# Performance work log

Hardware: AMD Instinct MI355X
Metric: run time of the kernel (lower is better)

## Reference

```python
import jax, jax.numpy as jnp
import numpy as np

# dims
H = 2048      # hidden_size
NH = 16       # num q heads
NKV = 8       # num kv heads
D = 128       # head_dim
E = 16        # routed experts
K = 4         # top_k
I = 1024      # moe_intermediate_size (per routed expert)
SI = 1024     # shared expert intermediate (moe_intermediate * num_shared)
T = 2048      # tokens
EPS = 1e-5
THETA = 10000.0
RSF = 1.0     # router_scaling_factor


def setup_inputs() -> dict:
    key = jax.random.key(0)
    ks = jax.random.split(key, 10)
    s = 0.02
    return {
        "positions": jnp.arange(T, dtype=jnp.int32),
        "hidden_states": jax.random.normal(ks[0], (T, H), jnp.float32),
        "qkv_w": jax.random.normal(ks[1], (H, (NH + 2 * NKV) * D), jnp.float32) * s,
        "o_w": jax.random.normal(ks[2], (NH * D, H), jnp.float32) * s,
        "q_norm_w": jnp.ones((D,), jnp.float32),
        "k_norm_w": jnp.ones((D,), jnp.float32),
        "ln1_w": jnp.ones((H,), jnp.float32),
        "ln2_w": jnp.ones((H,), jnp.float32),
        "gate_w": jax.random.normal(ks[3], (H, E), jnp.float32) * s,
        "expert_bias": jax.random.normal(ks[4], (E,), jnp.float32) * 0.1,
        "shared_gu_w": jax.random.normal(ks[5], (H, 2 * SI), jnp.float32) * s,
        "shared_down_w": jax.random.normal(ks[6], (SI, H), jnp.float32) * s,
        "exp_gu_w": jax.random.normal(ks[7], (E, H, 2 * I), jnp.float32) * s,
        "exp_down_w": jax.random.normal(ks[8], (E, I, H), jnp.float32) * s,
    }


def _rmsnorm(x, w):
    v = jnp.mean(x * x, axis=-1, keepdims=True)
    return x * jax.lax.rsqrt(v + EPS) * w


def _rope(x, cos, sin):
    # neox style: rotate halves. x: [T, heads, D]; cos/sin: [T, 1, D//2]
    x1, x2 = x[..., : D // 2], x[..., D // 2 :]
    return jnp.concatenate([x1 * cos - x2 * sin, x2 * cos + x1 * sin], axis=-1)


def reference(positions, hidden_states, qkv_w, o_w, q_norm_w, k_norm_w,
              ln1_w, ln2_w, gate_w, expert_bias, shared_gu_w, shared_down_w,
              exp_gu_w, exp_down_w):
    hs = hidden_states
    # --- attention block ---
    x = _rmsnorm(hs, ln1_w)
    qkv = x @ qkv_w
    q = qkv[:, : NH * D].reshape(T, NH, D)
    k = qkv[:, NH * D : NH * D + NKV * D].reshape(T, NKV, D)
    v = qkv[:, NH * D + NKV * D :].reshape(T, NKV, D)
    # per-head qk RMSNorm
    q = _rmsnorm(q, q_norm_w)
    k = _rmsnorm(k, k_norm_w)
    # rotary embedding
    inv_freq = 1.0 / (THETA ** (jnp.arange(0, D, 2, dtype=jnp.float32) / D))
    ang = positions.astype(jnp.float32)[:, None] * inv_freq  # [T, D/2]
    cos = jnp.cos(ang)[:, None, :]
    sin = jnp.sin(ang)[:, None, :]
    q = _rope(q, cos, sin)
    k = _rope(k, cos, sin)
    # GQA: repeat kv heads
    rep = NH // NKV
    k = jnp.repeat(k, rep, axis=1)  # [T, NH, D]
    v = jnp.repeat(v, rep, axis=1)
    scores = jnp.einsum('qhd,khd->hqk', q, k) * (D ** -0.5)
    causal = jnp.tril(jnp.ones((T, T), dtype=bool))
    scores = jnp.where(causal[None], scores, -1e30)
    attn = jax.nn.softmax(scores, axis=-1)
    ao = jnp.einsum('hqk,khd->qhd', attn, v).reshape(T, NH * D)
    h = hs + ao @ o_w
    # --- MoE block ---
    x2 = _rmsnorm(h, ln2_w)
    router_logits = x2 @ gate_w  # fp32 gate
    sig = jax.nn.sigmoid(router_logits)
    biased = sig + expert_bias  # correction bias only used for selection
    _, top_idx = jax.lax.top_k(biased, K)  # [T, K]
    w = jnp.take_along_axis(sig, top_idx, axis=-1)
    w = w / jnp.sum(w, axis=-1, keepdims=True) * RSF  # renormalize + routed scaling
    combine = jnp.sum(jax.nn.one_hot(top_idx, E, dtype=x2.dtype) * w[..., None], axis=1)  # [T, E]
    # routed experts (dense-masked reference for the grouped GEMM)
    gu = jnp.einsum('th,ehi->eti', x2, exp_gu_w)  # [E, T, 2I]
    act = jax.nn.silu(gu[..., :I]) * gu[..., I:]
    routed = jnp.einsum('eti,eih->eth', act, exp_down_w)
    routed = jnp.einsum('eth,te->th', routed, combine)
    # shared expert
    sgu = x2 @ shared_gu_w
    shared = (jax.nn.silu(sgu[:, :SI]) * sgu[:, SI:]) @ shared_down_w
    return h + routed + shared
```

## Files before the change

### kernel.cpp

```cpp
#include <hip/hip_runtime.h>
#include <math.h>

#define T_ 2048
#define H_ 2048
#define NH_ 16
#define NKV_ 8
#define D_ 128
#define E_ 16
#define I_ 1024
#define SI_ 1024

typedef _Float16 half8 __attribute__((ext_vector_type(8)));
typedef _Float16 half4_t __attribute__((ext_vector_type(4)));
typedef float f32x4 __attribute__((ext_vector_type(4)));

#define MFMA32(a,b,c) __builtin_amdgcn_mfma_f32_16x16x32_f16((a),(b),(c),0,0,0)

__device__ __constant__ float LO_S = 2048.0f;
__device__ __constant__ float LO_I = 1.0f/2048.0f;
#define EPS_ 1e-5f

#define GL16(gp, lp) __builtin_amdgcn_global_load_lds( \
    (const __attribute__((address_space(1))) unsigned int*)(const void*)(gp), \
    (__attribute__((address_space(3))) unsigned int*)(void*)(lp), 16, 0, 0)

__global__ void tables_k(const int* __restrict__ pos, float* __restrict__ cosT, float* __restrict__ sinT) {
  int t = blockIdx.x;
  int j = threadIdx.x;
  float pf = (float)pow(10000.0, (double)j / 64.0);
  float invf = 1.0f / pf;
  float ang = (float)pos[t] * invf;
  cosT[t*64 + j] = (float)cos((double)ang);
  sinT[t*64 + j] = (float)sin((double)ang);
}

__global__ __launch_bounds__(256) void rmsnorm_k(const float* __restrict__ x, const float* __restrict__ w,
                                                 _Float16* __restrict__ oh, _Float16* __restrict__ ol) {
  int row = blockIdx.x;
  const float* xr = x + (size_t)row * H_;
  int tid = threadIdx.x;
  float4 a = *(const float4*)(xr + tid*8);
  float4 b = *(const float4*)(xr + tid*8 + 4);
  float ss = a.x*a.x + a.y*a.y + a.z*a.z + a.w*a.w + b.x*b.x + b.y*b.y + b.z*b.z + b.w*b.w;
  #pragma unroll
  for (int m = 1; m < 64; m <<= 1) ss += __shfl_xor(ss, m);
  __shared__ float wsum[4];
  int wid = tid >> 6, lane = tid & 63;
  if (lane == 0) wsum[wid] = ss;
  __syncthreads();
  float tot = wsum[0] + wsum[1] + wsum[2] + wsum[3];
  float rinv = 1.0f / sqrtf(tot / (float)H_ + EPS_);
  const float* av = (const float*)&a;
  const float* bv = (const float*)&b;
  #pragma unroll
  for (int j = 0; j < 8; ++j) {
    float xv = (j < 4) ? av[j] : bv[j-4];
    float val = xv * rinv * w[tid*8 + j];
    _Float16 h = (_Float16)val;
    size_t o = (size_t)row*H_ + tid*8 + j;
    oh[o] = h;
    ol[o] = (_Float16)((val - (float)h) * LO_S);
  }
}

__global__ __launch_bounds__(128) void qkvpost_k(
    const float* __restrict__ qkv, const float* __restrict__ qnw, const float* __restrict__ knw,
    const float* __restrict__ cosT, const float* __restrict__ sinT,
    _Float16* __restrict__ qh, _Float16* __restrict__ ql,
    _Float16* __restrict__ kh, _Float16* __restrict__ kl,
    _Float16* __restrict__ vth, _Float16* __restrict__ vtl) {
  int t = blockIdx.x, u = blockIdx.y, d = threadIdx.x;
  float val = qkv[(size_t)t*4096 + u*128 + d];
  __shared__ float sv[128];
  __shared__ float ssum[2];
  if (u < 24) {
    float ss = val * val;
    #pragma unroll
    for (int m = 1; m < 64; m <<= 1) ss += __shfl_xor(ss, m);
    if ((d & 63) == 0) ssum[d >> 6] = ss;
    __syncthreads();
    float rinv = 1.0f / sqrtf((ssum[0] + ssum[1]) / 128.0f + EPS_);
    const float* nw = (u < 16) ? qnw : knw;
    float nv = val * rinv * nw[d];
    sv[d] = nv;
    __syncthreads();
    int j = d & 63;
    float c = cosT[t*64 + j], s = sinT[t*64 + j];
    float x1 = sv[j], x2 = sv[j + 64];
    float o = (d < 64) ? (x1*c - x2*s) : (x2*c + x1*s);
    _Float16 hv = (_Float16)o;
    _Float16 lv = (_Float16)((o - (float)hv) * LO_S);
    if (u < 16) { size_t off = ((size_t)u*T_ + t)*D_ + d; qh[off] = hv; ql[off] = lv; }
    else { size_t off = ((size_t)(u-16)*T_ + t)*D_ + d; kh[off] = hv; kl[off] = lv; }
  } else {
    int kv = u - 24;
    _Float16 hv = (_Float16)val;
    _Float16 lv = (_Float16)((val - (float)hv) * LO_S);
    size_t off = ((size_t)kv*D_ + d)*T_ + t;
    vth[off] = hv; vtl[off] = lv;
  }
}

template<bool SPL>
__global__ __launch_bounds__(256) void transpose_k(const float* __restrict__ in, _Float16* __restrict__ oh,
                                                   _Float16* __restrict__ ol, int R, int C) {
  size_t zo = (size_t)blockIdx.z * R * C;
  in += zo; oh += zo; if (SPL) ol += zo;
  __shared__ float tile[32][33];
  int c0 = blockIdx.x*32, r0 = blockIdx.y*32;
  int tid = threadIdx.x;
  int lr = tid >> 3;
  int lc = (tid & 7) * 4;
  float4 v = *(const float4*)(in + (size_t)(r0+lr)*C + c0 + lc);
  tile[lr][lc+0]=v.x; tile[lr][lc+1]=v.y; tile[lr][lc+2]=v.z; tile[lr][lc+3]=v.w;
  __syncthreads();
  half4_t hv, lv;
  #pragma unroll
  for (int j = 0; j < 4; ++j) {
    float f = tile[lc+j][lr];
    _Float16 h = (_Float16)f;
    hv[j] = h;
    if (SPL) lv[j] = (_Float16)((f - (float)h) * LO_S);
  }
  size_t ob = (size_t)(c0+lr)*R + r0 + lc;
  *(half4_t*)(oh + ob) = hv;
  if (SPL) *(half4_t*)(ol + ob) = lv;
}

__global__ __launch_bounds__(256) void transpose_gu_k(const float* __restrict__ in, _Float16* __restrict__ out,
                                                      int R, int Ih) {
  size_t zi = (size_t)blockIdx.z * R * 2 * Ih;
  in += zi; out += zi;
  __shared__ float tg[32][17], tu[32][17];
  int j0 = blockIdx.x*16, h0 = blockIdx.y*32;
  int tid = threadIdx.x;
  int lh = tid >> 3;
  int lj = (tid & 7) * 2;
  int C = 2*Ih;
  float2 g = *(const float2*)(in + (size_t)(h0+lh)*C + j0 + lj);
  float2 u = *(const float2*)(in + (size_t)(h0+lh)*C + Ih + j0 + lj);
  tg[lh][lj]=g.x; tg[lh][lj+1]=g.y; tu[lh][lj]=u.x; tu[lh][lj+1]=u.y;
  __syncthreads();
  int orow = tid >> 3;
  int oj = orow >> 1, op = orow & 1;
  int oc = (tid & 7) * 4;
  float (*sel)[17] = op ? tu : tg;
  half4_t pack;
  #pragma unroll
  for (int q = 0; q < 4; ++q) pack[q] = (_Float16)sel[oc+q][oj];
  *(half4_t*)(out + (size_t)(2*(j0+oj)+op)*R + h0 + oc) = pack;
}

__global__ __launch_bounds__(256) void attn_k(
    const _Float16* __restrict__ qh_, const _Float16* __restrict__ ql_,
    const _Float16* __restrict__ kh_, const _Float16* __restrict__ kl_,
    const _Float16* __restrict__ vh_, const _Float16* __restrict__ vl_,
    _Float16* __restrict__ aoh, _Float16* __restrict__ aol) {
  __shared__ _Float16 sK [2][4096];
  __shared__ _Float16 sKl[2][4096];
  __shared__ _Float16 sV [2][4096];
  __shared__ _Float16 sVl[2][4096];
  const int head = blockIdx.x;
  const int pair = blockIdx.y;
  const int kvh = head >> 1;
  const int wid = threadIdx.x >> 6, lane = threadIdx.x & 63;
  const int fr = lane & 15, fs = lane >> 4;
  const float scale = 0.08838834764831845f;

  const char* kbC  = (const char*)(kh_ + (size_t)kvh*T_*D_);
  const char* kbCl = (const char*)(kl_ + (size_t)kvh*T_*D_);
  const char* vbC  = (const char*)(vh_ + (size_t)kvh*D_*T_);
  const char* vbCl = (const char*)(vl_ + (size_t)kvh*D_*T_);

  auto stage = [&](int buf, int kvt) {
    #pragma unroll
    for (int i = 0; i < 2; ++i) {
      const int off  = wid*2048 + i*1024;
      const int loff = off + lane*16;
      const int r  = loff >> 8;
      const int u  = (loff >> 4) & 15;
      const int us = u ^ (r & 7);
      const size_t gb = ((size_t)(kvt + r) << 8) + ((size_t)us << 4);
      GL16(kbC  + gb, (char*)&sK [buf][0] + off);
      GL16(kbCl + gb, (char*)&sKl[buf][0] + off);
      const int d   = loff >> 6;
      const int uv  = (loff >> 4) & 3;
      const int uvs = uv ^ (d & 3);
      const size_t gvb = (size_t)d*(T_*2) + (size_t)kvt*2 + ((size_t)uvs << 4);
      GL16(vbC  + gvb, (char*)&sV [buf][0] + off);
      GL16(vbCl + gvb, (char*)&sVl[buf][0] + off);
    }
  };

  #pragma unroll 1
  for (int halfT = 0; halfT < 2; ++halfT) {
    const int tile = halfT == 0 ? (31 - pair) : pair;
    const int q0 = tile*64 + wid*16;
    const int qrow = q0 + fr;
    const _Float16* qb_  = qh_ + ((size_t)head*T_ + qrow)*D_;
    const _Float16* qlb_ = ql_ + ((size_t)head*T_ + qrow)*D_;
    half8 qf[4], qfl[4];
    #pragma unroll
    for (int s = 0; s < 4; ++s) {
      qf[s]  = *(const half8*)(qb_  + s*32 + fs*8);
      qfl[s] = *(const half8*)(qlb_ + s*32 + fs*8);
    }
    float m = -1e30f, lsum = 0.f;
    f32x4 oacc[8] = {};
    f32x4 oacc2[8] = {};
    const int nc = 2*tile + 2;

    stage(0, 0);
    #pragma unroll 1
    for (int c = 0; c < nc; ++c) {
      const int kvt = c*32;
      const int buf = c & 1;
      __syncthreads();
      if (c + 1 < nc) stage(buf ^ 1, kvt + 32);

      f32x4 sa = {0,0,0,0}, sa2 = {0,0,0,0}, sb = {0,0,0,0}, sb2 = {0,0,0,0};
      __builtin_amdgcn_s_setprio(1);
      #pragma unroll
      for (int s = 0; s < 4; ++s) {
        const int rA = fr, rB = fr + 16;
        const int eA = (((4*s + fs) ^ (rA & 7)) << 3);
        const int eB = (((4*s + fs) ^ (rB & 7)) << 3);
        half8 kfA  = *(const half8*)&sK [buf][rA*128 + eA];
        half8 kflA = *(const half8*)&sKl[buf][rA*128 + eA];
        half8 kfB  = *(const half8*)&sK [buf][rB*128 + eB];
        half8 kflB = *(const half8*)&sKl[buf][rB*128 + eB];
        sa  = MFMA32(kfA, qf[s], sa);
        sa2 = MFMA32(kfA, qfl[s], sa2);
        sa2 = MFMA32(kflA, qf[s], sa2);
        sb  = MFMA32(kfB, qf[s], sb);
        sb2 = MFMA32(kfB, qfl[s], sb2);
        sb2 = MFMA32(kflB, qf[s], sb2);
      }
      __builtin_amdgcn_s_setprio(0);

      float sv[8];
      #pragma unroll
      for (int r = 0; r < 4; ++r) {
        float xA = (sa[r] + sa2[r]*LO_I) * scale;
        sv[r] = (kvt + fs*4 + r > qrow) ? -INFINITY : xA;
        float xB = (sb[r] + sb2[r]*LO_I) * scale;
        sv[4+r] = (kvt + 16 + fs*4 + r > qrow) ? -INFINITY : xB;
      }
      float tm = -INFINITY;
      #pragma unroll
      for (int j = 0; j < 8; ++j) tm = fmaxf(tm, sv[j]);
      tm = fmaxf(tm, __shfl_xor(tm, 16));
      tm = fmaxf(tm, __shfl_xor(tm, 32));
      float mnew = fmaxf(m, tm);
      float p[8]; float ps = 0.f;
      #pragma unroll
      for (int j = 0; j < 8; ++j) { p[j] = __expf(sv[j] - mnew); ps += p[j]; }
      ps += __shfl_xor(ps, 16);
      ps += __shfl_xor(ps, 32);
      if (mnew > m) {
        float f = __expf(m - mnew);
        lsum *= f;
        #pragma unroll
        for (int db = 0; db < 8; ++db) { oacc[db] *= f; oacc2[db] *= f; }
        m = mnew;
      }
      lsum += ps;
      half8 ph, pl;
      #pragma unroll
      for (int j = 0; j < 8; ++j) {
        _Float16 hp = (_Float16)p[j];
        ph[j] = hp;
        pl[j] = (_Float16)((p[j] - (float)hp) * LO_S);
      }

      __builtin_amdgcn_s_setprio(1);
      #pragma unroll
      for (int db = 0; db < 8; ++db) {
        const int d0 = db*16 + fr;
        const int base = d0*32;
        const int e1 = ((((fs>>1)    ) ^ (d0 & 3)) << 3) + (fs & 1)*4;
        const int e2 = (((2 + (fs>>1)) ^ (d0 & 3)) << 3) + (fs & 1)*4;
        half4_t v0  = *(const half4_t*)&sV [buf][base + e1];
        half4_t v1  = *(const half4_t*)&sV [buf][base + e2];
        half4_t v0l = *(const half4_t*)&sVl[buf][base + e1];
        half4_t v1l = *(const half4_t*)&sVl[buf][base + e2];
        half8 vf, vfl;
        #pragma unroll
        for (int j = 0; j < 4; ++j) { vf[j] = v0[j]; vf[4+j] = v1[j]; vfl[j] = v0l[j]; vfl[4+j] = v1l[j]; }
        oacc[db]  = MFMA32(vf, ph, oacc[db]);
        oacc2[db] = MFMA32(vf, pl, oacc2[db]);
        oacc2[db] = MFMA32(vfl, ph, oacc2[db]);
      }
      __builtin_amdgcn_s_setprio(0);
    }
    __syncthreads();

    float inv = 1.0f / lsum;
    #pragma unroll
    for (int db = 0; db < 8; ++db) {
      #pragma unroll
      for (int r = 0; r < 4; ++r) {
        float val = (oacc[db][r] + oacc2[db][r]*LO_I) * inv;
        int dd = db*16 + fs*4 + r;
        size_t off = (size_t)qrow*(NH_*D_) + head*D_ + dd;
        _Float16 hv = (_Float16)val;
        aoh[off] = hv;
        aol[off] = (_Float16)((val - (float)hv) * LO_S);
      }
    }
  }
}

__global__ __launch_bounds__(256) void router_k(const _Float16* __restrict__ x2h, const _Float16* __restrict__ x2l,
    const float* __restrict__ gw, const float* __restrict__ eb,
    int* __restrict__ cnt, int* __restrict__ list, float* __restrict__ wl) {
  int t = blockIdx.x*4 + (threadIdx.x >> 6);
  int lane = threadIdx.x & 63;
  const _Float16* xh = x2h + (size_t)t*H_;
  const _Float16* xl = x2l + (size_t)t*H_;
  f32x4 a0 = {0,0,0,0}, a1 = {0,0,0,0}, a2 = {0,0,0,0}, a3 = {0,0,0,0};
  for (int h = lane; h < H_; h += 64) {
    float xv = (float)xh[h] + (float)xl[h] * LO_I;
    const float* g = gw + (size_t)h*16;
    a0 += xv * (*(const f32x4*)(g));
    a1 += xv * (*(const f32x4*)(g+4));
    a2 += xv * (*(const f32x4*)(g+8));
    a3 += xv * (*(const f32x4*)(g+12));
  }
  float acc[16];
  #pragma unroll
  for (int j = 0; j < 4; ++j) { acc[j]=a0[j]; acc[4+j]=a1[j]; acc[8+j]=a2[j]; acc[12+j]=a3[j]; }
  #pragma unroll
  for (int mm = 1; mm < 64; mm <<= 1) {
    #pragma unroll
    for (int e2 = 0; e2 < 16; ++e2) acc[e2] += __shfl_xor(acc[e2], mm);
  }
  if (lane == 0) {
    float sig[16], biased[16];
    #pragma unroll
    for (int e2 = 0; e2 < 16; ++e2) {
      float s = 1.0f / (1.0f + expf(-acc[e2]));
      sig[e2] = s; biased[e2] = s + eb[e2];
    }
    int sel[4]; float wv[4]; float wsum = 0.f;
    unsigned used = 0;
    for (int j = 0; j < 4; ++j) {
      int bi = -1; float bv = -1e30f;
      for (int e2 = 0; e2 < 16; ++e2)
        if (!((used >> e2) & 1) && biased[e2] > bv) { bv = biased[e2]; bi = e2; }
      used |= 1u << bi;
      sel[j] = bi; wv[j] = sig[bi]; wsum += sig[bi];
    }
    for (int j = 0; j < 4; ++j) {
      int e2 = sel[j];
      int pos = atomicAdd(&cnt[e2], 1);
      list[e2*T_ + pos] = t;
      wl[e2*T_ + pos] = wv[j] / wsum;
    }
  }
}

__global__ void scan_k(const int* __restrict__ cnt, int* __restrict__ base) {
  if (threadIdx.x == 0 && blockIdx.x == 0) {
    int s = 0;
    for (int e2 = 0; e2 < 16; ++e2) { base[e2] = s; s += cnt[e2]; }
  }
}

struct GArgs {
  const _Float16* Ah; const _Float16* Al;
  const _Float16* Bh; const _Float16* Bl;
  int M, N, K;
  const int* rowlist; const float* wlist; const int* cnt; const int* base;
  float* C; const float* res; _Float16* act; float* outAt; int ldc;
};

template<int MODE, bool SPLIT, int DEPTH>
__global__ __launch_bounds__(256) void gemm_k(GArgs p) {
  constexpr int LPS = SPLIT ? 8 : 4;
  const int e = blockIdx.z;
  const int M = p.cnt ? p.cnt[e] : p.M;
  const int m0 = blockIdx.y * 128;
  if (m0 >= M) return;
  const int n0 = blockIdx.x * 128;
  const int tid = threadIdx.x;
  const int wid = tid >> 6, lane = tid & 63;

  __shared__ _Float16 sA[DEPTH][4096];
  __shared__ _Float16 sB[DEPTH][4096];
  __shared__ _Float16 sAl[SPLIT ? DEPTH : 1][SPLIT ? 4096 : 8];
  __shared__ _Float16 sBl[SPLIT ? DEPTH : 1][SPLIT ? 4096 : 8];

  const char* aPtr[2]; const char* alPtr[2];
  const char* bPtr[2]; const char* blPtr[2];
  int ldsOff[2];
  #pragma unroll
  for (int i = 0; i < 2; ++i) {
    const int u = (i*4 + wid)*64 + lane;
    const int row = u >> 2;
    const int slot = ((u & 3) ^ (row & 3)) * 16;
    ldsOff[i] = (i*4 + wid) * 1024;
    size_t aIdx;
    if constexpr (MODE == 2) {
      if (p.rowlist) {
        int tok = p.rowlist[(size_t)e * T_ + m0 + row];
        tok = tok < 0 ? 0 : (tok > T_ - 1 ? T_ - 1 : tok);
        aIdx = (size_t)tok;
      } else aIdx = (size_t)(m0 + row);
    } else if constexpr (MODE == 3) {
      aIdx = (size_t)p.base[e] + m0 + row;
    } else {
      aIdx = (size_t)(m0 + row);
    }
    aPtr[i] = (const char*)(p.Ah + aIdx * (size_t)p.K) + slot;
    if constexpr (SPLIT) alPtr[i] = (const char*)(p.Al + aIdx * (size_t)p.K) + slot;
    const size_t bIdx = (size_t)e * p.N + n0 + row;
    bPtr[i] = (const char*)(p.Bh + bIdx * (size_t)p.K) + slot;
    if constexpr (SPLIT) blPtr[i] = (const char*)(p.Bl + bIdx * (size_t)p.K) + slot;
  }

  auto stage = [&](int buf, int kb) {
    #pragma unroll
    for (int i = 0; i < 2; ++i) {
      GL16(aPtr[i] + kb, (char*)&sA[buf][0] + ldsOff[i]);
      GL16(bPtr[i] + kb, (char*)&sB[buf][0] + ldsOff[i]);
      if constexpr (SPLIT) {
        GL16(alPtr[i] + kb, (char*)&sAl[buf][0] + ldsOff[i]);
        GL16(blPtr[i] + kb, (char*)&sBl[buf][0] + ldsOff[i]);
      }
    }
  };

  const int wr = (wid >> 1) * 64, wc = (wid & 1) * 64;
  const int fr = lane & 15, fs = lane >> 4;

  f32x4 acc[4][4] = {};
  f32x4 acc2[4][4] = {};

  const int nt = p.K >> 5;
  stage(0, 0);
  if constexpr (DEPTH == 3) { if (nt > 1) stage(1, 64); }

  for (int t = 0; t < nt; ++t) {
    if constexpr (DEPTH == 3) {
      if (t + 2 < nt) stage((t + 2) % 3, (t + 2) * 64);
      __builtin_amdgcn_sched_barrier(0);
      if (t + 2 < nt)      asm volatile("s_waitcnt vmcnt(%0)" :: "i"(2*LPS) : "memory");
      else if (t + 1 < nt) asm volatile("s_waitcnt vmcnt(%0)" :: "i"(LPS)   : "memory");
      else                 asm volatile("s_waitcnt vmcnt(0)" ::: "memory");
    } else {
      if (t + 1 < nt) {
        stage((t + 1) & 1, (t + 1) * 64);
        __builtin_amdgcn_sched_barrier(0);
        asm volatile("s_waitcnt vmcnt(%0)" :: "i"(LPS) : "memory");
      } else {
        __builtin_amdgcn_sched_barrier(0);
        asm volatile("s_waitcnt vmcnt(0)" ::: "memory");
      }
    }
    __builtin_amdgcn_s_barrier();
    __builtin_amdgcn_sched_barrier(0);

    const int cb = (DEPTH == 3) ? (t % 3) : (t & 1);
    half8 ah[4], bh[4], al[4], bl[4];
    #pragma unroll
    for (int i = 0; i < 4; ++i) {
      const int pa = (fs ^ ((wr + i*16 + fr) & 3)) * 8;
      const int pb = (fs ^ ((wc + i*16 + fr) & 3)) * 8;
      ah[i] = *(const half8*)&sA[cb][(wr + i*16 + fr)*32 + pa];
      bh[i] = *(const half8*)&sB[cb][(wc + i*16 + fr)*32 + pb];
      if constexpr (SPLIT) {
        al[i] = *(const half8*)&sAl[cb][(wr + i*16 + fr)*32 + pa];
        bl[i] = *(const half8*)&sBl[cb][(wc + i*16 + fr)*32 + pb];
      }
    }
    __builtin_amdgcn_s_setprio(1);
    #pragma unroll
    for (int mi = 0; mi < 4; ++mi) {
      #pragma unroll
      for (int ni = 0; ni < 4; ++ni) {
        acc[mi][ni] = MFMA32(ah[mi], bh[ni], acc[mi][ni]);
        if constexpr (SPLIT) {
          acc2[mi][ni] = MFMA32(ah[mi], bl[ni], acc2[mi][ni]);
          acc2[mi][ni] = MFMA32(al[mi], bh[ni], acc2[mi][ni]);
        }
      }
    }
    __builtin_amdgcn_s_setprio(0);
    __builtin_amdgcn_sched_barrier(0);
    __builtin_amdgcn_s_barrier();
    __builtin_amdgcn_sched_barrier(0);
  }

  const int actld = p.N >> 1;
  #pragma unroll
  for (int mi = 0; mi < 4; ++mi) {
    #pragma unroll
    for (int ni = 0; ni < 4; ++ni) {
      f32x4 v4 = acc[mi][ni];
      if constexpr (SPLIT) v4 = v4 + acc2[mi][ni] * LO_I;
      const int colb = n0 + wc + ni*16 + fr;
      #pragma unroll
      for (int r = 0; r < 4; ++r) {
        const int row = m0 + wr + mi*16 + fs*4 + r;
        float val = v4[r];
        if constexpr (MODE == 0) {
          if (row < M) p.C[(size_t)row * p.ldc + colb] = val;
        } else if constexpr (MODE == 1) {
          if (row < M) p.C[(size_t)row * p.ldc + colb] = p.res[(size_t)row * p.ldc + colb] + val;
        } else if constexpr (MODE == 2) {
          float other = __shfl_xor(val, 1);
          float g = (fr & 1) ? other : val;
          float u = (fr & 1) ? val : other;
          float a = g / (1.0f + expf(-g)) * u;
          if (!(fr & 1) && row < M) {
            size_t ar = (size_t)(p.base ? p.base[e] : 0) + row;
            p.act[ar * (size_t)actld + (colb >> 1)] = (_Float16)a;
          }
        } else {
          if (row < M) {
            int tok = p.rowlist[(size_t)e * T_ + row];
            float w = p.wlist[(size_t)e * T_ + row];
            atomicAdd(&p.outAt[(size_t)tok * p.ldc + colb], val * w);
          }
        }
      }
    }
  }
}

extern "C" void kernel_launch(void* const* d_in, const int* in_sizes, int n_in,
                              void* d_out, int out_size, void* d_ws, size_t ws_size,
                              hipStream_t stream) {
  (void)in_sizes; (void)n_in; (void)out_size; (void)ws_size;
  const int*   positions = (const int*)  d_in[0];
  const float* hidden    = (const float*)d_in[1];
  const float* qkv_w     = (const float*)d_in[2];
  const float* o_w       = (const float*)d_in[3];
  const float* q_norm_w  = (const float*)d_in[4];
  const float* k_norm_w  = (const float*)d_in[5];
  const float* ln1_w     = (const float*)d_in[6];
  const float* ln2_w     = (const float*)d_in[7];
  const float* gate_w    = (const float*)d_in[8];
  const float* ebias     = (const float*)d_in[9];
  const float* sgu_w     = (const float*)d_in[10];
  const float* sdown_w   = (const float*)d_in[11];
  const float* egu_w     = (const float*)d_in[12];
  const float* edown_w   = (const float*)d_in[13];
  float* out = (float*)d_out;

  char* wsp = (char*)d_ws;
  size_t off = 0;
  auto alloc = [&](size_t bytes) -> void* {
    void* p = wsp + off;
    off = (off + bytes + 255) & ~(size_t)255;
    return p;
  };
  float*    cosT   = (float*)   alloc((size_t)T_*64*4);
  float*    sinT   = (float*)   alloc((size_t)T_*64*4);
  _Float16* x_h    = (_Float16*)alloc((size_t)T_*H_*2);
  _Float16* x_l    = (_Float16*)alloc((size_t)T_*H_*2);
  float*    qkvb   = (float*)   alloc((size_t)T_*4096*4);
  _Float16* q_h    = (_Float16*)alloc((size_t)NH_*T_*D_*2);
  _Float16* q_l    = (_Float16*)alloc((size_t)NH_*T_*D_*2);
  _Float16* k_h    = (_Float16*)alloc((size_t)NKV_*T_*D_*2);
  _Float16* k_l    = (_Float16*)alloc((size_t)NKV_*T_*D_*2);
  _Float16* vt_h   = (_Float16*)alloc((size_t)NKV_*T_*D_*2);
  _Float16* vt_l   = (_Float16*)alloc((size_t)NKV_*T_*D_*2);
  _Float16* ao_h   = (_Float16*)alloc((size_t)T_*NH_*D_*2);
  _Float16* ao_l   = (_Float16*)alloc((size_t)T_*NH_*D_*2);
  float*    hbuf   = (float*)   alloc((size_t)T_*H_*4);
  _Float16* x2_h   = (_Float16*)alloc((size_t)T_*H_*2);
  _Float16* x2_l   = (_Float16*)alloc((size_t)T_*H_*2);
  _Float16* qkvwT_h= (_Float16*)alloc((size_t)4096*H_*2);
  _Float16* qkvwT_l= (_Float16*)alloc((size_t)4096*H_*2);
  _Float16* owT_h  = (_Float16*)alloc((size_t)H_*H_*2);
  _Float16* owT_l  = (_Float16*)alloc((size_t)H_*H_*2);
  _Float16* sguT   = (_Float16*)alloc((size_t)2*SI_*H_*2);
  _Float16* sdownT = (_Float16*)alloc((size_t)H_*SI_*2);
  _Float16* eguT   = (_Float16*)alloc((size_t)E_*2*I_*H_*2);
  _Float16* edownT = (_Float16*)alloc((size_t)E_*H_*I_*2);
  _Float16* act_s  = (_Float16*)alloc((size_t)T_*SI_*2);
  _Float16* act_e  = (_Float16*)alloc((size_t)(T_*4 + 512)*I_*2);
  int*   cnt   = (int*)  alloc(E_*4);
  int*   ebase = (int*)  alloc(E_*4);
  int*   list  = (int*)  alloc((size_t)E_*T_*4);
  float* wlst  = (float*)alloc((size_t)E_*T_*4);

  hipMemsetAsync(cnt, 0, E_*4, stream);
  tables_k<<<T_, 64, 0, stream>>>(positions, cosT, sinT);

  transpose_k<true ><<<dim3(4096/32, H_/32, 1), 256, 0, stream>>>(qkv_w, qkvwT_h, qkvwT_l, H_, 4096);
  transpose_k<true ><<<dim3(H_/32,  H_/32, 1), 256, 0, stream>>>(o_w, owT_h, owT_l, H_, H_);
  transpose_gu_k    <<<dim3(SI_/16, H_/32, 1), 256, 0, stream>>>(sgu_w, sguT, H_, SI_);
  transpose_k<false><<<dim3(H_/32, SI_/32, 1), 256, 0, stream>>>(sdown_w, sdownT, nullptr, SI_, H_);
  transpose_gu_k    <<<dim3(I_/16,  H_/32, E_), 256, 0, stream>>>(egu_w, eguT, H_, I_);
  transpose_k<false><<<dim3(H_/32,  I_/32, E_), 256, 0, stream>>>(edown_w, edownT, nullptr, I_, H_);

  rmsnorm_k<<<T_, 256, 0, stream>>>(hidden, ln1_w, x_h, x_l);

  { GArgs g{}; g.Ah=x_h; g.Al=x_l; g.Bh=qkvwT_h; g.Bl=qkvwT_l; g.M=T_; g.N=4096; g.K=H_;
    g.C=qkvb; g.ldc=4096;
    gemm_k<0,true,2><<<dim3(4096/128, T_/128, 1), 256, 0, stream>>>(g); }

  qkvpost_k<<<dim3(T_, 32, 1), 128, 0, stream>>>(qkvb, q_norm_w, k_norm_w, cosT, sinT,
                                                 q_h, q_l, k_h, k_l, vt_h, vt_l);

  attn_k<<<dim3(NH_, 16), 256, 0, stream>>>(q_h, q_l, k_h, k_l, vt_h, vt_l, ao_h, ao_l);

  { GArgs g{}; g.Ah=ao_h; g.Al=ao_l; g.Bh=owT_h; g.Bl=owT_l; g.M=T_; g.N=H_; g.K=H_;
    g.C=hbuf; g.res=hidden; g.ldc=H_;
    gemm_k<1,true,2><<<dim3(H_/128, T_/128, 1), 256, 0, stream>>>(g); }

  rmsnorm_k<<<T_, 256, 0, stream>>>(hbuf, ln2_w, x2_h, x2_l);

  router_k<<<T_/4, 256, 0, stream>>>(x2_h, x2_l, gate_w, ebias, cnt, list, wlst);
  scan_k<<<1, 64, 0, stream>>>(cnt, ebase);

  { GArgs g{}; g.Ah=x2_h; g.Bh=sguT; g.M=T_; g.N=2*SI_; g.K=H_; g.act=act_s;
    gemm_k<2,false,3><<<dim3(2*SI_/128, T_/128, 1), 256, 0, stream>>>(g); }

  { GArgs g{}; g.Ah=act_s; g.Bh=sdownT; g.M=T_; g.N=H_; g.K=SI_;
    g.C=out; g.res=hbuf; g.ldc=H_;
    gemm_k<1,false,3><<<dim3(H_/128, T_/128, 1), 256, 0, stream>>>(g); }

  { GArgs g{}; g.Ah=x2_h; g.Bh=eguT; g.M=T_; g.N=2*I_; g.K=H_;
    g.rowlist=list; g.cnt=cnt; g.base=ebase; g.act=act_e;
    gemm_k<2,false,3><<<dim3(2*I_/128, T_/128, E_), 256, 0, stream>>>(g); }

  { GArgs g{}; g.Ah=act_e; g.Bh=edownT; g.M=T_; g.N=H_; g.K=I_;
    g.rowlist=list; g.wlist=wlst; g.cnt=cnt; g.base=ebase;
    g.outAt=out; g.ldc=H_;
    gemm_k<3,false,3><<<dim3(H_/128, T_/128, E_), 256, 0, stream>>>(g); }
}
```

Baseline: 1.202 ms.

## Use 512-thread GEMM blocks with 8 waves each computing 64x32 subtiles

The shared GEMM kernel now runs 8 waves per 128x128 tile instead of 4. Each wave computes a 64x32 subtile, which halves its accumulator registers, and each thread issues one staged load per operand instead of two. Launch bounds are raised to 512 threads with a minimum of 4 blocks, so more waves can be resident to hide latency. The cost is that each wave reuses fewer B fragments per A fragment, so there are more LDS reads per MFMA and more barrier participants.

```diff
diff --git a/kernel.cpp b/kernel.cpp
--- a/kernel.cpp
+++ b/kernel.cpp
@@ -376,8 +376,8 @@
 };
 
 template<int MODE, bool SPLIT, int DEPTH>
-__global__ __launch_bounds__(256) void gemm_k(GArgs p) {
-  constexpr int LPS = SPLIT ? 8 : 4;
+__global__ __launch_bounds__(512, 4) void gemm_k(GArgs p) {
+  constexpr int LPS = SPLIT ? 4 : 2;
   const int e = blockIdx.z;
   const int M = p.cnt ? p.cnt[e] : p.M;
   const int m0 = blockIdx.y * 128;
@@ -391,51 +391,41 @@
   __shared__ _Float16 sAl[SPLIT ? DEPTH : 1][SPLIT ? 4096 : 8];
   __shared__ _Float16 sBl[SPLIT ? DEPTH : 1][SPLIT ? 4096 : 8];
 
-  const char* aPtr[2]; const char* alPtr[2];
-  const char* bPtr[2]; const char* blPtr[2];
-  int ldsOff[2];
-  #pragma unroll
-  for (int i = 0; i < 2; ++i) {
-    const int u = (i*4 + wid)*64 + lane;
-    const int row = u >> 2;
-    const int slot = ((u & 3) ^ (row & 3)) * 16;
-    ldsOff[i] = (i*4 + wid) * 1024;
-    size_t aIdx;
-    if constexpr (MODE == 2) {
-      if (p.rowlist) {
-        int tok = p.rowlist[(size_t)e * T_ + m0 + row];
-        tok = tok < 0 ? 0 : (tok > T_ - 1 ? T_ - 1 : tok);
-        aIdx = (size_t)tok;
-      } else aIdx = (size_t)(m0 + row);
-    } else if constexpr (MODE == 3) {
-      aIdx = (size_t)p.base[e] + m0 + row;
-    } else {
-      aIdx = (size_t)(m0 + row);
-    }
-    aPtr[i] = (const char*)(p.Ah + aIdx * (size_t)p.K) + slot;
-    if constexpr (SPLIT) alPtr[i] = (const char*)(p.Al + aIdx * (size_t)p.K) + slot;
-    const size_t bIdx = (size_t)e * p.N + n0 + row;
-    bPtr[i] = (const char*)(p.Bh + bIdx * (size_t)p.K) + slot;
-    if constexpr (SPLIT) blPtr[i] = (const char*)(p.Bl + bIdx * (size_t)p.K) + slot;
-  }
+  const int srow = tid >> 2;
+  const int slot = ((tid & 3) ^ (srow & 3)) * 16;
+  const int ldsOff = wid * 1024;
+  size_t aIdx;
+  if constexpr (MODE == 2) {
+    if (p.rowlist) {
+      int tok = p.rowlist[(size_t)e * T_ + m0 + srow];
+      tok = tok < 0 ? 0 : (tok > T_ - 1 ? T_ - 1 : tok);
+      aIdx = (size_t)tok;
+    } else aIdx = (size_t)(m0 + srow);
+  } else if constexpr (MODE == 3) {
+    aIdx = (size_t)p.base[e] + m0 + srow;
+  } else {
+    aIdx = (size_t)(m0 + srow);
+  }
+  const char* aPtr  = (const char*)(p.Ah + aIdx * (size_t)p.K) + slot;
+  const char* alPtr = SPLIT ? (const char*)(p.Al + aIdx * (size_t)p.K) + slot : aPtr;
+  const size_t bIdx = (size_t)e * p.N + n0 + srow;
+  const char* bPtr  = (const char*)(p.Bh + bIdx * (size_t)p.K) + slot;
+  const char* blPtr = SPLIT ? (const char*)(p.Bl + bIdx * (size_t)p.K) + slot : bPtr;
 
   auto stage = [&](int buf, int kb) {
-    #pragma unroll
-    for (int i = 0; i < 2; ++i) {
-      GL16(aPtr[i] + kb, (char*)&sA[buf][0] + ldsOff[i]);
-      GL16(bPtr[i] + kb, (char*)&sB[buf][0] + ldsOff[i]);
-      if constexpr (SPLIT) {
-        GL16(alPtr[i] + kb, (char*)&sAl[buf][0] + ldsOff[i]);
-        GL16(blPtr[i] + kb, (char*)&sBl[buf][0] + ldsOff[i]);
-      }
+    GL16(aPtr + kb, (char*)&sA[buf][0] + ldsOff);
+    GL16(bPtr + kb, (char*)&sB[buf][0] + ldsOff);
+    if constexpr (SPLIT) {
+      GL16(alPtr + kb, (char*)&sAl[buf][0] + ldsOff);
+      GL16(blPtr + kb, (char*)&sBl[buf][0] + ldsOff);
     }
   };
 
-  const int wr = (wid >> 1) * 64, wc = (wid & 1) * 64;
+  const int wr = (wid >> 2) * 64, wc = (wid & 3) * 32;
   const int fr = lane & 15, fs = lane >> 4;
 
-  f32x4 acc[4][4] = {};
-  f32x4 acc2[4][4] = {};
+  f32x4 acc[4][2] = {};
+  f32x4 acc2[4][2] = {};
 
   const int nt = p.K >> 5;
   stage(0, 0);
@@ -462,23 +452,24 @@
     __builtin_amdgcn_sched_barrier(0);
 
     const int cb = (DEPTH == 3) ? (t % 3) : (t & 1);
-    half8 ah[4], bh[4], al[4], bl[4];
+    half8 ah[4], bh[2], al[4], bl[2];
     #pragma unroll
     for (int i = 0; i < 4; ++i) {
       const int pa = (fs ^ ((wr + i*16 + fr) & 3)) * 8;
+      ah[i] = *(const half8*)&sA[cb][(wr + i*16 + fr)*32 + pa];
+      if constexpr (SPLIT) al[i] = *(const half8*)&sAl[cb][(wr + i*16 + fr)*32 + pa];
+    }
+    #pragma unroll
+    for (int i = 0; i < 2; ++i) {
       const int pb = (fs ^ ((wc + i*16 + fr) & 3)) * 8;
-      ah[i] = *(const half8*)&sA[cb][(wr + i*16 + fr)*32 + pa];
       bh[i] = *(const half8*)&sB[cb][(wc + i*16 + fr)*32 + pb];
-      if constexpr (SPLIT) {
-        al[i] = *(const half8*)&sAl[cb][(wr + i*16 + fr)*32 + pa];
-        bl[i] = *(const half8*)&sBl[cb][(wc + i*16 + fr)*32 + pb];
-      }
+      if constexpr (SPLIT) bl[i] = *(const half8*)&sBl[cb][(wc + i*16 + fr)*32 + pb];
     }
     __builtin_amdgcn_s_setprio(1);
     #pragma unroll
     for (int mi = 0; mi < 4; ++mi) {
       #pragma unroll
-      for (int ni = 0; ni < 4; ++ni) {
+      for (int ni = 0; ni < 2; ++ni) {
         acc[mi][ni] = MFMA32(ah[mi], bh[ni], acc[mi][ni]);
         if constexpr (SPLIT) {
           acc2[mi][ni] = MFMA32(ah[mi], bl[ni], acc2[mi][ni]);
@@ -496,7 +487,7 @@
   #pragma unroll
   for (int mi = 0; mi < 4; ++mi) {
     #pragma unroll
-    for (int ni = 0; ni < 4; ++ni) {
+    for (int ni = 0; ni < 2; ++ni) {
       f32x4 v4 = acc[mi][ni];
       if constexpr (SPLIT) v4 = v4 + acc2[mi][ni] * LO_I;
       const int colb = n0 + wc + ni*16 + fr;
@@ -601,7 +592,7 @@
 
   { GArgs g{}; g.Ah=x_h; g.Al=x_l; g.Bh=qkvwT_h; g.Bl=qkvwT_l; g.M=T_; g.N=4096; g.K=H_;
     g.C=qkvb; g.ldc=4096;
-    gemm_k<0,true,2><<<dim3(4096/128, T_/128, 1), 256, 0, stream>>>(g); }
+    gemm_k<0,true,2><<<dim3(4096/128, T_/128, 1), 512, 0, stream>>>(g); }
 
   qkvpost_k<<<dim3(T_, 32, 1), 128, 0, stream>>>(qkvb, q_norm_w, k_norm_w, cosT, sinT,
                                                  q_h, q_l, k_h, k_l, vt_h, vt_l);
@@ -610,7 +601,7 @@
 
   { GArgs g{}; g.Ah=ao_h; g.Al=ao_l; g.Bh=owT_h; g.Bl=owT_l; g.M=T_; g.N=H_; g.K=H_;
     g.C=hbuf; g.res=hidden; g.ldc=H_;
-    gemm_k<1,true,2><<<dim3(H_/128, T_/128, 1), 256, 0, stream>>>(g); }
+    gemm_k<1,true,2><<<dim3(H_/128, T_/128, 1), 512, 0, stream>>>(g); }
 
   rmsnorm_k<<<T_, 256, 0, stream>>>(hbuf, ln2_w, x2_h, x2_l);
 
@@ -618,18 +609,18 @@
   scan_k<<<1, 64, 0, stream>>>(cnt, ebase);
 
   { GArgs g{}; g.Ah=x2_h; g.Bh=sguT; g.M=T_; g.N=2*SI_; g.K=H_; g.act=act_s;
-    gemm_k<2,false,3><<<dim3(2*SI_/128, T_/128, 1), 256, 0, stream>>>(g); }
+    gemm_k<2,false,3><<<dim3(2*SI_/128, T_/128, 1), 512, 0, stream>>>(g); }
 
   { GArgs g{}; g.Ah=act_s; g.Bh=sdownT; g.M=T_; g.N=H_; g.K=SI_;
     g.C=out; g.res=hbuf; g.ldc=H_;
-    gemm_k<1,false,3><<<dim3(H_/128, T_/128, 1), 256, 0, stream>>>(g); }
+    gemm_k<1,false,3><<<dim3(H_/128, T_/128, 1), 512, 0, stream>>>(g); }
 
   { GArgs g{}; g.Ah=x2_h; g.Bh=eguT; g.M=T_; g.N=2*I_; g.K=H_;
     g.rowlist=list; g.cnt=cnt; g.base=ebase; g.act=act_e;
-    gemm_k<2,false,3><<<dim3(2*I_/128, T_/128, E_), 256, 0, stream>>>(g); }
+    gemm_k<2,false,3><<<dim3(2*I_/128, T_/128, E_), 512, 0, stream>>>(g); }
 
   { GArgs g{}; g.Ah=act_e; g.Bh=edownT; g.M=T_; g.N=H_; g.K=I_;
     g.rowlist=list; g.wlist=wlst; g.cnt=cnt; g.base=ebase;
     g.outAt=out; g.ldc=H_;
-    gemm_k<3,false,3><<<dim3(H_/128, T_/128, E_), 256, 0, stream>>>(g); }
-}
+    gemm_k<3,false,3><<<dim3(H_/128, T_/128, E_), 512, 0, stream>>>(g); }
+}
```

Measured after the change: 1.060 ms. 11.8% less time.
